# Performance work log

Hardware: AMD Instinct MI355X
Metric: run time of the kernel (lower is better)

The kernel has to match this reference:

```python
import jax, jax.numpy as jnp
import numpy as np

B, C, H, W = 2, 128, 64, 64
EPS = 1e-5


def setup_inputs() -> dict:
    key = jax.random.key(0)
    ks = jax.random.split(key, 8)
    sc = 1.0 / np.sqrt(C)
    inp = {
        "x": jax.random.normal(ks[0], (B, C, H, W, 2), jnp.float32),
        # naive complex BN affine params: per-channel, per-component (real/imag)
        "bn_w": jnp.ones((C, 2), jnp.float32),
        "bn_b": jnp.zeros((C, 2), jnp.float32),
        # complex 1x1 conv weights: (out_c, in_c, 2) -> [..,0]=W_real, [..,1]=W_imag
        "wq": jax.random.normal(ks[1], (C, C, 2), jnp.float32) * sc,
        "bq": jnp.zeros((C, 2), jnp.float32),
        "wk": jax.random.normal(ks[2], (C, C, 2), jnp.float32) * sc,
        "bk": jnp.zeros((C, 2), jnp.float32),
        "wv": jax.random.normal(ks[3], (C, C, 2), jnp.float32) * sc,
        "bv": jnp.zeros((C, 2), jnp.float32),
        "gamma": jnp.float32(0.05),
    }
    return inp


def _complex_bn(x, w, b):
    # naive complex BN: normalize real and imag independently per channel
    # x: (B,C,H,W,2); stats over (B,H,W) per (C, component)
    mean = x.mean(axis=(0, 2, 3), keepdims=True)
    var = x.var(axis=(0, 2, 3), keepdims=True)
    xn = (x - mean) * jax.lax.rsqrt(var + EPS)
    return xn * w[None, :, None, None, :] + b[None, :, None, None, :]


def _complex_conv1x1(x, w, b):
    # x: (B,C,H,W,2); w: (O,C,2); b: (O,2)
    xr, xi = x[..., 0], x[..., 1]
    wr, wi = w[..., 0], w[..., 1]
    yr = jnp.einsum('oc,bchw->bohw', wr, xr) - jnp.einsum('oc,bchw->bohw', wi, xi)
    yi = jnp.einsum('oc,bchw->bohw', wr, xi) + jnp.einsum('oc,bchw->bohw', wi, xr)
    yr = yr + b[:, 0][None, :, None, None]
    yi = yi + b[:, 1][None, :, None, None]
    return jnp.stack([yr, yi], axis=-1)


def _attention(x, wq, bq, wk, bk, wv, bv, gamma):
    scale = C ** (-0.5)
    N = H * W
    # q,k,v: (B,C,H,W,2) -> (B,C,N,2) -> (B,N,C,2)
    to_tokens = lambda t: t.reshape(B, C, N, 2).transpose(0, 2, 1, 3)
    q = to_tokens(_complex_conv1x1(x, wq, bq))
    k = to_tokens(_complex_conv1x1(x, wk, bk))
    v = to_tokens(_complex_conv1x1(x, wv, bv))

    qr, qi = q[..., 0], q[..., 1]          # (B,N,C)
    kr, ki = k[..., 0], -k[..., 1]         # conjugate of k
    # k_t = conj(k) with token/channel axes swapped -> (B,C,N)
    ktr = kr.transpose(0, 2, 1)
    kti = ki.transpose(0, 2, 1)

    # complex matmul q @ k_t -> only the real part is used downstream
    attn_real = jnp.einsum('bnc,bcm->bnm', qr, ktr) - jnp.einsum('bnc,bcm->bnm', qi, kti)
    attn_w = jax.nn.softmax(attn_real * scale, axis=-1)  # (B,N,N)
    # dropout = identity (eval mode)

    # attn is purely real -> complex matmul reduces to two real matmuls
    out_r = jnp.einsum('bnm,bmc->bnc', attn_w, v[..., 0])
    out_i = jnp.einsum('bnm,bmc->bnc', attn_w, v[..., 1])
    out = jnp.stack([out_r, out_i], axis=-1)              # (B,N,C,2)
    out = out.transpose(0, 2, 1, 3).reshape(B, C, H, W, 2)
    return x + gamma * out


def reference(x, bn_w, bn_b, wq, bq, wk, bk, wv, bv, gamma):
    xn = _complex_bn(x, bn_w, bn_b)
    return _attention(xn, wq, bq, wk, bk, wv, bv, gamma)
```

## Files before the change

kernel.cpp:

```cpp
#include <hip/hip_runtime.h>
#include <hip/hip_bf16.h>
#include <hip/hip_fp8.h>

typedef __bf16 bf16_t;
typedef __bf16 bf16x8 __attribute__((ext_vector_type(8)));
typedef float  f32x4  __attribute__((ext_vector_type(4)));
typedef long   i64_t;

#define MFMA16(A,B,C) __builtin_amdgcn_mfma_f32_16x16x32_bf16((A),(B),(C),0,0,0)
#define MFMA8(A,B,C)  __builtin_amdgcn_mfma_f32_16x16x32_fp8_fp8((A),(B),(C),0,0,0)
#define MFMA85(A,B,C) __builtin_amdgcn_mfma_f32_16x16x32_bf8_fp8((A),(B),(C),0,0,0)

constexpr int Bn = 2, Cc = 128, Hh = 64, Wd = 64;
constexpr int N  = Hh * Wd;
constexpr int T  = Bn * N;
constexpr int D  = 2 * Cc;
constexpr int NSP = 8;
constexpr float EPS = 1e-5f;
constexpr float SCL = 0.08838834764831845f * 1.4426950408889634f;
constexpr float PSH = 9.0f;

__device__ __forceinline__ int tfrag(int row, int ch) {
    return (((ch >> 5) * 4 + (row >> 4)) << 10) +
           ((((ch >> 3) & 3) * 16 + (row & 15)) << 4) + (ch & 7) * 2;
}
__device__ __forceinline__ int tfrag8(int row, int ch) {
    return (((ch >> 5) * 4 + (row >> 4)) << 9) +
           ((((ch >> 3) & 3) * 16 + (row & 15)) << 3) + (ch & 7);
}
__device__ __forceinline__ int vfrag8(int ch, int key) {
    return (((key >> 5) * 16 + (ch >> 4)) << 9) +
           ((((key >> 3) & 3) * 16 + (ch & 15)) << 3) + (key & 7);
}

__device__ __forceinline__ void gl16(const void* g, void* l) {
    __builtin_amdgcn_global_load_lds(
        (const __attribute__((address_space(1))) void*)g,
        (__attribute__((address_space(3))) void*)l, 16, 0, 0);
}

__global__ void k_pre(const float* __restrict__ x, float4* __restrict__ part,
                      const float* __restrict__ wq, const float* __restrict__ wk,
                      const float* __restrict__ wv, const float* __restrict__ bq,
                      const float* __restrict__ bk, const float* __restrict__ bv,
                      char* __restrict__ Wg, float* __restrict__ bt) {
    int tid = threadIdx.x;
    if (blockIdx.x < 512) {
        int bid = blockIdx.x;
        int q = bid >> 7, c = bid & 127;
        float sr = 0.f, si = 0.f, qr = 0.f, qi = 0.f;
        for (int b = 0; b < Bn; ++b) {
            const float2* p = (const float2*)x + (size_t)(b * Cc + c) * N + q * 1024;
            for (int i = tid; i < 1024; i += 256) {
                float2 v = p[i];
                sr += v.x; si += v.y; qr += v.x * v.x; qi += v.y * v.y;
            }
        }
        #pragma unroll
        for (int d = 32; d >= 1; d >>= 1) {
            sr += __shfl_xor(sr, d); si += __shfl_xor(si, d);
            qr += __shfl_xor(qr, d); qi += __shfl_xor(qi, d);
        }
        __shared__ float red[4][4];
        int w = tid >> 6;
        if ((tid & 63) == 0) { red[w][0] = sr; red[w][1] = si; red[w][2] = qr; red[w][3] = qi; }
        __syncthreads();
        if (tid == 0) {
            part[c * 4 + q] = make_float4(red[0][0] + red[1][0] + red[2][0] + red[3][0],
                                          red[0][1] + red[1][1] + red[2][1] + red[3][1],
                                          red[0][2] + red[1][2] + red[2][2] + red[3][2],
                                          red[0][3] + red[1][3] + red[2][3] + red[3][3]);
        }
    } else {
        int o = blockIdx.x - 512;
        int k = tid;
        int proj = o >> 8, oc = o & 255;
        const float* wsrc = proj == 0 ? wq : (proj == 1 ? wk : wv);
        const float* bsrc = proj == 0 ? bq : (proj == 1 ? bk : bv);
        int co = oc >> 7, oo = oc & 127;
        int c = k & 127, kc = k >> 7;
        float val;
        if (co == 0) val = (kc == 0) ? wsrc[(oo * 128 + c) * 2 + 0] : -wsrc[(oo * 128 + c) * 2 + 1];
        else         val = (kc == 0) ? wsrc[(oo * 128 + c) * 2 + 1] :  wsrc[(oo * 128 + c) * 2 + 0];
        int tile = o >> 6, row = o & 63;
        *(bf16_t*)(Wg + (size_t)tile * 32768 + tfrag(row, k)) = (bf16_t)val;
        if (k == 0) bt[o] = bsrc[oo * 2 + co];
    }
}

__global__ void k_norm(const float* __restrict__ x, const float4* __restrict__ part,
                       const float* __restrict__ bn_w, const float* __restrict__ bn_b,
                       char* __restrict__ XNg) {
    __shared__ float4 ssl[128];
    __shared__ __align__(16) char Tsh[32768];
    int blk = blockIdx.x;
    int b = blk >> 6, hw0 = (blk & 63) * 64;
    int tid = threadIdx.x;
    if (tid < 128) {
        float4 p0 = part[tid * 4 + 0], p1 = part[tid * 4 + 1];
        float4 p2 = part[tid * 4 + 2], p3 = part[tid * 4 + 3];
        float sr = p0.x + p1.x + p2.x + p3.x, si = p0.y + p1.y + p2.y + p3.y;
        float qr = p0.z + p1.z + p2.z + p3.z, qi = p0.w + p1.w + p2.w + p3.w;
        const float inv = 1.0f / (float)(Bn * N);
        float mr = sr * inv, mi = si * inv;
        float vr = qr * inv - mr * mr, vi = qi * inv - mi * mi;
        float scr = bn_w[tid * 2 + 0] * rsqrtf(vr + EPS);
        float sci = bn_w[tid * 2 + 1] * rsqrtf(vi + EPS);
        ssl[tid] = make_float4(scr, bn_b[tid * 2 + 0] - mr * scr,
                               sci, bn_b[tid * 2 + 1] - mi * sci);
    }
    __syncthreads();
    const float2* xin = (const float2*)x;
    #pragma unroll
    for (int it = 0; it < 32; ++it) {
        int idx = it * 256 + tid;
        int c = idx >> 6, hw = idx & 63;
        size_t gi = (size_t)(b * Cc + c) * N + hw0 + hw;
        float2 v = xin[gi];
        float4 s = ssl[c];
        *(bf16_t*)(Tsh + tfrag(hw, c))       = (bf16_t)(v.x * s.x + s.y);
        *(bf16_t*)(Tsh + tfrag(hw, c + 128)) = (bf16_t)(v.y * s.z + s.w);
    }
    __syncthreads();
    #pragma unroll
    for (int it = 0; it < 8; ++it) {
        int idx = it * 256 + tid;
        *(uint4*)(XNg + (size_t)blk * 32768 + idx * 16) = *(const uint4*)(Tsh + idx * 16);
    }
}

__global__ __launch_bounds__(256) void k_qkv(const char* __restrict__ XNg,
        const char* __restrict__ Wg, const float* __restrict__ bt,
        char* __restrict__ Qg, char* __restrict__ Kg, char* __restrict__ Vg) {
    __shared__ __align__(16) char Xsh[32768];
    __shared__ __align__(16) char Wsh[32768];
    int mx = blockIdx.x, ny = blockIdx.y;
    int tid = threadIdx.x;
    int w = tid >> 6, lane = tid & 63, n15 = lane & 15, quad = lane >> 4;
    const char* xs = XNg + (size_t)mx * 32768;
    const char* wsp = Wg + (size_t)ny * 32768;
    #pragma unroll
    for (int i = 0; i < 8; ++i) {
        int off = (w * 8 + i) * 1024 + lane * 16;
        gl16(xs + off, Xsh + off);
        gl16(wsp + off, Wsh + off);
    }
    __syncthreads();
    f32x4 acc[4] = {};
    #pragma unroll
    for (int ks = 0; ks < 8; ++ks) {
        bf16x8 a = *(const bf16x8*)(Xsh + (ks * 4 + w) * 1024 + lane * 16);
        #pragma unroll
        for (int t = 0; t < 4; ++t) {
            bf16x8 bw = *(const bf16x8*)(Wsh + (ks * 4 + t) * 1024 + lane * 16);
            acc[t] = MFMA16(a, bw, acc[t]);
        }
    }
    int proj = ny >> 2;
    int jb = (ny & 3) * 64;
    #pragma unroll
    for (int t = 0; t < 4; ++t) {
        int j = jb + t * 16 + n15;
        float bias = bt[ny * 64 + t * 16 + n15];
        unsigned w01 = (unsigned)__builtin_amdgcn_cvt_pk_fp8_f32(
            acc[t][0] + bias, acc[t][1] + bias, 0, false);
        unsigned w23 = (unsigned)__builtin_amdgcn_cvt_pk_fp8_f32(
            acc[t][2] + bias, acc[t][3] + bias, 0, false);
        #pragma unroll
        for (int r = 0; r < 4; ++r) {
            int tk = mx * 64 + w * 16 + quad * 4 + r;
            unsigned char v8 = (unsigned char)((r < 2 ? (w01 >> (8 * r))
                                                      : (w23 >> (8 * (r - 2)))) & 0xff);
            int bb = tk >> 12, n = tk & (N - 1);
            if (proj == 0) {
                *(unsigned char*)(Qg + (size_t)(tk >> 6) * 16384 + tfrag8(tk & 63, j)) = v8;
            } else {
                size_t tb = (size_t)(bb * 64 + (n >> 6)) * 16384;
                if (proj == 1) *(unsigned char*)(Kg + tb + tfrag8(n & 63, j)) = v8;
                else           *(unsigned char*)(Vg + tb + vfrag8(j, n & 63)) = v8;
            }
        }
    }
}

__global__ __launch_bounds__(256, 4) void k_attn(const char* __restrict__ Qg,
        const char* __restrict__ Kg, const char* __restrict__ Vg,
        bf16_t* __restrict__ Opb, float* __restrict__ Lp) {
    __shared__ __align__(16) char Ksh[16384];
    __shared__ __align__(16) char Vsh[16384];
    __shared__ __align__(16) char Psh[4096];
    int bid = blockIdx.x;
    int grp = bid & 15, qt = bid >> 4;
    int sp = grp & 7, b = grp >> 3;
    int tid = threadIdx.x;
    int w = tid >> 6, lane = tid & 63, n15 = lane & 15, quad = lane >> 4;
    int r = w >> 1, h = w & 1;

    const i64_t ONES = 0x3838383838383838L;

    i64_t qf[2][8];
    const char* qb = Qg + (size_t)(b * 64 + qt) * 16384;
    #pragma unroll
    for (int g = 0; g < 2; ++g)
        #pragma unroll
        for (int ks = 0; ks < 8; ++ks)
            qf[g][ks] = *(const i64_t*)(qb + ((ks * 4 + r * 2 + g) << 9) + lane * 8);

    f32x4 o[2][8] = {};
    f32x4 l_[2] = {};

    for (int kt = 0; kt < 8; ++kt) {
        size_t tb = (size_t)(b * 64 + sp * 8 + kt) * 16384;
        __syncthreads();
        #pragma unroll
        for (int i = 0; i < 4; ++i) {
            int off = (w * 4 + i) * 1024 + lane * 16;
            gl16(Kg + tb + off, Ksh + off);
            gl16(Vg + tb + off, Vsh + off);
        }
        __syncthreads();

        f32x4 s[2][2] = {};
        #pragma unroll
        for (int ks = 0; ks < 8; ++ks) {
            #pragma unroll
            for (int c = 0; c < 2; ++c) {
                i64_t kf = *(const i64_t*)(Ksh + ((ks * 4 + h * 2 + c) << 9) + lane * 8);
                s[0][c] = MFMA8(qf[0][ks], kf, s[0][c]);
                s[1][c] = MFMA8(qf[1][ks], kf, s[1][c]);
            }
        }
        #pragma unroll
        for (int g = 0; g < 2; ++g)
            #pragma unroll
            for (int c = 0; c < 2; ++c) {
                float p0 = __builtin_amdgcn_exp2f(s[g][c][0] * SCL - PSH);
                float p1 = __builtin_amdgcn_exp2f(s[g][c][1] * SCL - PSH);
                float p2 = __builtin_amdgcn_exp2f(s[g][c][2] * SCL - PSH);
                float p3 = __builtin_amdgcn_exp2f(s[g][c][3] * SCL - PSH);
                unsigned w01 = (unsigned)__builtin_amdgcn_cvt_pk_bf8_f32(p0, p1, 0, false);
                unsigned w23 = (unsigned)__builtin_amdgcn_cvt_pk_bf8_f32(p2, p3, 0, false);
                char* pb = Psh + ((h * 4 + r * 2 + g) << 9) +
                           (((c * 2 + (n15 >> 3)) * 16 + quad * 4) << 3) + (n15 & 7);
                pb[0]  = (unsigned char)(w01 & 0xff);
                pb[8]  = (unsigned char)((w01 >> 8) & 0xff);
                pb[16] = (unsigned char)(w23 & 0xff);
                pb[24] = (unsigned char)((w23 >> 8) & 0xff);
            }
        __syncthreads();

        #pragma unroll
        for (int k2 = 0; k2 < 2; ++k2) {
            i64_t pa0 = *(const i64_t*)(Psh + ((k2 * 4 + r * 2 + 0) << 9) + lane * 8);
            i64_t pa1 = *(const i64_t*)(Psh + ((k2 * 4 + r * 2 + 1) << 9) + lane * 8);
            l_[0] = MFMA85(pa0, ONES, l_[0]);
            l_[1] = MFMA85(pa1, ONES, l_[1]);
            #pragma unroll
            for (int ct = 0; ct < 8; ++ct) {
                i64_t vf = *(const i64_t*)(Vsh + ((k2 * 16 + h * 8 + ct) << 9) + lane * 8);
                o[0][ct] = MFMA85(pa0, vf, o[0][ct]);
                o[1][ct] = MFMA85(pa1, vf, o[1][ct]);
            }
        }
    }
    int tok0 = b * N + qt * 64 + r * 32;
    #pragma unroll
    for (int g = 0; g < 2; ++g) {
        #pragma unroll
        for (int ct = 0; ct < 8; ++ct)
            #pragma unroll
            for (int ri = 0; ri < 4; ++ri)
                Opb[((size_t)sp * T + tok0 + g * 16 + quad * 4 + ri) * D +
                    h * 128 + ct * 16 + n15] = (bf16_t)o[g][ct][ri];
        if (h == 0 && n15 == 0) {
            #pragma unroll
            for (int ri = 0; ri < 4; ++ri)
                Lp[sp * T + tok0 + g * 16 + quad * 4 + ri] = l_[g][ri];
        }
    }
}

__global__ void k_comb(const bf16_t* __restrict__ Opb, const float* __restrict__ Lp,
                       const float4* __restrict__ part, const float* __restrict__ bn_w,
                       const float* __restrict__ bn_b, const float* __restrict__ x,
                       const float* __restrict__ gamma, float* __restrict__ out) {
    __shared__ float4 ssl[128];
    __shared__ float wts[32];
    __shared__ float Ot[256 * 33];
    int blk = blockIdx.x;
    int b = blk >> 7, hw0 = (blk & 127) * 32;
    int tok0 = b * N + hw0;
    int tid = threadIdx.x;
    if (tid < 128) {
        float4 p0 = part[tid * 4 + 0], p1 = part[tid * 4 + 1];
        float4 p2 = part[tid * 4 + 2], p3 = part[tid * 4 + 3];
        float sr = p0.x + p1.x + p2.x + p3.x, si = p0.y + p1.y + p2.y + p3.y;
        float qr = p0.z + p1.z + p2.z + p3.z, qi = p0.w + p1.w + p2.w + p3.w;
        const float inv = 1.0f / (float)(Bn * N);
        float mr = sr * inv, mi = si * inv;
        float vr = qr * inv - mr * mr, vi = qi * inv - mi * mi;
        float scr = bn_w[tid * 2 + 0] * rsqrtf(vr + EPS);
        float sci = bn_w[tid * 2 + 1] * rsqrtf(vi + EPS);
        ssl[tid] = make_float4(scr, bn_b[tid * 2 + 0] - mr * scr,
                               sci, bn_b[tid * 2 + 1] - mi * sci);
    }
    if (tid < 32) {
        float Z = 0.f;
        #pragma unroll
        for (int s = 0; s < NSP; ++s) Z += Lp[s * T + tok0 + tid];
        wts[tid] = gamma[0] / Z;
    }
    __syncthreads();
    #pragma unroll
    for (int i = 0; i < 4; ++i) {
        int idx = i * 256 + tid;
        int tk = idx >> 5, chunk = idx & 31;
        size_t base = (size_t)(tok0 + tk) * D + chunk * 8;
        float acc[8] = {};
        #pragma unroll
        for (int s = 0; s < NSP; ++s) {
            bf16x8 v = *(const bf16x8*)(Opb + (size_t)s * T * D + base);
            #pragma unroll
            for (int j = 0; j < 8; ++j) acc[j] += (float)v[j];
        }
        float ww = wts[tk];
        #pragma unroll
        for (int j = 0; j < 8; ++j) Ot[(chunk * 8 + j) * 33 + tk] = acc[j] * ww;
    }
    __syncthreads();
    const float2* xin = (const float2*)x;
    float2* xo = (float2*)out;
    #pragma unroll
    for (int i = 0; i < 16; ++i) {
        int linear = i * 256 + tid;
        int c = linear >> 5, hwo = linear & 31;
        size_t idx = (size_t)(b * Cc + c) * N + hw0 + hwo;
        float2 v = xin[idx];
        float4 s = ssl[c];
        float2 res;
        res.x = v.x * s.x + s.y + Ot[c * 33 + hwo];
        res.y = v.y * s.z + s.w + Ot[(128 + c) * 33 + hwo];
        xo[idx] = res;
    }
}

extern "C" void kernel_launch(void* const* d_in, const int* in_sizes, int n_in,
                              void* d_out, int out_size, void* d_ws, size_t ws_size,
                              hipStream_t stream) {
    const float* x    = (const float*)d_in[0];
    const float* bn_w = (const float*)d_in[1];
    const float* bn_b = (const float*)d_in[2];
    const float* wq   = (const float*)d_in[3];
    const float* bq   = (const float*)d_in[4];
    const float* wk   = (const float*)d_in[5];
    const float* bk   = (const float*)d_in[6];
    const float* wv   = (const float*)d_in[7];
    const float* bv   = (const float*)d_in[8];
    const float* gam  = (const float*)d_in[9];
    float* out = (float*)d_out;

    char* ws = (char*)d_ws;
    size_t off = 0;
    auto alloc = [&](size_t bytes) -> void* {
        void* p = ws + off;
        off += (bytes + 255) & ~(size_t)255;
        return p;
    };
    float4* part = (float4*)alloc(512 * sizeof(float4));
    char*   XNg  = (char*)alloc((size_t)128 * 32768);
    char*   Wg   = (char*)alloc((size_t)12 * 32768);
    float*  bt   = (float*)alloc(768 * 4);
    char*   Qg   = (char*)alloc((size_t)128 * 16384);
    char*   Kg   = (char*)alloc((size_t)128 * 16384);
    char*   Vg   = (char*)alloc((size_t)128 * 16384);
    bf16_t* Opb  = (bf16_t*)alloc((size_t)NSP * T * D * 2);
    float*  Lp   = (float*)alloc((size_t)NSP * T * 4);

    k_pre<<<1280, 256, 0, stream>>>(x, part, wq, wk, wv, bq, bk, bv, Wg, bt);
    k_norm<<<128, 256, 0, stream>>>(x, part, bn_w, bn_b, XNg);
    k_qkv<<<dim3(128, 12), 256, 0, stream>>>(XNg, Wg, bt, Qg, Kg, Vg);
    k_attn<<<1024, 256, 0, stream>>>(Qg, Kg, Vg, Opb, Lp);
    k_comb<<<256, 256, 0, stream>>>(Opb, Lp, part, bn_w, bn_b, x, gam, out);
}
```

Before: 149.7 us.

## Halve attention key splits, stage QKV stores in LDS, vectorize x loads

Reduces the key-dimension split count for attention from 8 to 4, so each attention block processes 16 key tiles and the combine kernel reads fewer partial outputs. The QKV projection now writes fp8 results into shared memory first and then emits coalesced 16-byte global stores, replacing scattered single-byte writes. The stats and normalization kernels load x as float4 instead of float2. The combine kernel is retiled to 16 tokens per block with 512 blocks. Fewer splits means fewer attention blocks (512), which lowers parallelism per wave but cuts partial-sum traffic.

```diff
diff --git a/kernel.cpp b/kernel.cpp
--- a/kernel.cpp
+++ b/kernel.cpp
@@ -15,7 +15,7 @@
 constexpr int N  = Hh * Wd;
 constexpr int T  = Bn * N;
 constexpr int D  = 2 * Cc;
-constexpr int NSP = 8;
+constexpr int NSP = 4;
 constexpr float EPS = 1e-5f;
 constexpr float SCL = 0.08838834764831845f * 1.4426950408889634f;
 constexpr float PSH = 9.0f;
@@ -23,14 +23,6 @@
 __device__ __forceinline__ int tfrag(int row, int ch) {
     return (((ch >> 5) * 4 + (row >> 4)) << 10) +
            ((((ch >> 3) & 3) * 16 + (row & 15)) << 4) + (ch & 7) * 2;
-}
-__device__ __forceinline__ int tfrag8(int row, int ch) {
-    return (((ch >> 5) * 4 + (row >> 4)) << 9) +
-           ((((ch >> 3) & 3) * 16 + (row & 15)) << 3) + (ch & 7);
-}
-__device__ __forceinline__ int vfrag8(int ch, int key) {
-    return (((key >> 5) * 16 + (ch >> 4)) << 9) +
-           ((((key >> 3) & 3) * 16 + (ch & 15)) << 3) + (key & 7);
 }
 
 __device__ __forceinline__ void gl16(const void* g, void* l) {
@@ -50,10 +42,12 @@
         int q = bid >> 7, c = bid & 127;
         float sr = 0.f, si = 0.f, qr = 0.f, qi = 0.f;
         for (int b = 0; b < Bn; ++b) {
-            const float2* p = (const float2*)x + (size_t)(b * Cc + c) * N + q * 1024;
-            for (int i = tid; i < 1024; i += 256) {
-                float2 v = p[i];
-                sr += v.x; si += v.y; qr += v.x * v.x; qi += v.y * v.y;
+            const float4* p = (const float4*)((const float2*)x +
+                              (size_t)(b * Cc + c) * N + q * 1024);
+            for (int i = tid; i < 512; i += 256) {
+                float4 v = p[i];
+                sr += v.x + v.z; si += v.y + v.w;
+                qr += v.x * v.x + v.z * v.z; qi += v.y * v.y + v.w * v.w;
             }
         }
         #pragma unroll
@@ -110,16 +104,18 @@
                                sci, bn_b[tid * 2 + 1] - mi * sci);
     }
     __syncthreads();
-    const float2* xin = (const float2*)x;
-    #pragma unroll
-    for (int it = 0; it < 32; ++it) {
+    const float4* xin4 = (const float4*)x;
+    #pragma unroll
+    for (int it = 0; it < 16; ++it) {
         int idx = it * 256 + tid;
-        int c = idx >> 6, hw = idx & 63;
-        size_t gi = (size_t)(b * Cc + c) * N + hw0 + hw;
-        float2 v = xin[gi];
+        int c = idx >> 5, h2 = (idx & 31) * 2;
+        size_t gi = ((size_t)(b * Cc + c) * N + hw0 + h2) >> 1;
+        float4 v = xin4[gi];
         float4 s = ssl[c];
-        *(bf16_t*)(Tsh + tfrag(hw, c))       = (bf16_t)(v.x * s.x + s.y);
-        *(bf16_t*)(Tsh + tfrag(hw, c + 128)) = (bf16_t)(v.y * s.z + s.w);
+        *(bf16_t*)(Tsh + tfrag(h2, c))           = (bf16_t)(v.x * s.x + s.y);
+        *(bf16_t*)(Tsh + tfrag(h2, c + 128))     = (bf16_t)(v.y * s.z + s.w);
+        *(bf16_t*)(Tsh + tfrag(h2 + 1, c))       = (bf16_t)(v.z * s.x + s.y);
+        *(bf16_t*)(Tsh + tfrag(h2 + 1, c + 128)) = (bf16_t)(v.w * s.z + s.w);
     }
     __syncthreads();
     #pragma unroll
@@ -158,28 +154,41 @@
     }
     int proj = ny >> 2;
     int jb = (ny & 3) * 64;
+    __syncthreads();
+    char* Osh = Xsh;
     #pragma unroll
     for (int t = 0; t < 4; ++t) {
-        int j = jb + t * 16 + n15;
         float bias = bt[ny * 64 + t * 16 + n15];
         unsigned w01 = (unsigned)__builtin_amdgcn_cvt_pk_fp8_f32(
             acc[t][0] + bias, acc[t][1] + bias, 0, false);
         unsigned w23 = (unsigned)__builtin_amdgcn_cvt_pk_fp8_f32(
             acc[t][2] + bias, acc[t][3] + bias, 0, false);
+        unsigned char vb[4] = {(unsigned char)(w01 & 0xff), (unsigned char)((w01 >> 8) & 0xff),
+                               (unsigned char)(w23 & 0xff), (unsigned char)((w23 >> 8) & 0xff)};
         #pragma unroll
         for (int r = 0; r < 4; ++r) {
-            int tk = mx * 64 + w * 16 + quad * 4 + r;
-            unsigned char v8 = (unsigned char)((r < 2 ? (w01 >> (8 * r))
-                                                      : (w23 >> (8 * (r - 2)))) & 0xff);
-            int bb = tk >> 12, n = tk & (N - 1);
-            if (proj == 0) {
-                *(unsigned char*)(Qg + (size_t)(tk >> 6) * 16384 + tfrag8(tk & 63, j)) = v8;
+            if (proj < 2) {
+                int lf  = (t >> 1) * 4 + w;
+                int lif = (((2 * t + (n15 >> 3)) & 3) << 4) + quad * 4 + r;
+                Osh[lf * 512 + lif * 8 + (n15 & 7)] = vb[r];
             } else {
-                size_t tb = (size_t)(bb * 64 + (n >> 6)) * 16384;
-                if (proj == 1) *(unsigned char*)(Kg + tb + tfrag8(n & 63, j)) = v8;
-                else           *(unsigned char*)(Vg + tb + vfrag8(j, n & 63)) = v8;
-            }
-        }
+                int key = w * 16 + quad * 4 + r;
+                int lf  = (w >> 1) * 4 + t;
+                int lif = (((key >> 3) & 3) << 4) + n15;
+                Osh[lf * 512 + lif * 8 + (key & 7)] = vb[r];
+            }
+        }
+    }
+    __syncthreads();
+    {
+        int lf = tid >> 5, sub = (tid & 31) * 16;
+        size_t tile = (proj == 0) ? (size_t)mx
+                                  : (size_t)((mx >> 6) * 64 + (mx & 63));
+        int gfrag = (proj < 2) ? ((jb >> 5) * 4 + lf)
+                               : ((lf >> 2) * 16 + (jb >> 4) + (lf & 3));
+        char* dst = (proj == 0 ? Qg : (proj == 1 ? Kg : Vg));
+        *(uint4*)(dst + tile * 16384 + (size_t)gfrag * 512 + sub) =
+            *(const uint4*)(Osh + tid * 16);
     }
 }
 
@@ -190,8 +199,8 @@
     __shared__ __align__(16) char Vsh[16384];
     __shared__ __align__(16) char Psh[4096];
     int bid = blockIdx.x;
-    int grp = bid & 15, qt = bid >> 4;
-    int sp = grp & 7, b = grp >> 3;
+    int grp = bid & 7, qt = bid >> 3;
+    int sp = grp & 3, b = grp >> 2;
     int tid = threadIdx.x;
     int w = tid >> 6, lane = tid & 63, n15 = lane & 15, quad = lane >> 4;
     int r = w >> 1, h = w & 1;
@@ -209,8 +218,8 @@
     f32x4 o[2][8] = {};
     f32x4 l_[2] = {};
 
-    for (int kt = 0; kt < 8; ++kt) {
-        size_t tb = (size_t)(b * 64 + sp * 8 + kt) * 16384;
+    for (int kt = 0; kt < 16; ++kt) {
+        size_t tb = (size_t)(b * 64 + sp * 16 + kt) * 16384;
         __syncthreads();
         #pragma unroll
         for (int i = 0; i < 4; ++i) {
@@ -285,10 +294,10 @@
                        const float* __restrict__ bn_b, const float* __restrict__ x,
                        const float* __restrict__ gamma, float* __restrict__ out) {
     __shared__ float4 ssl[128];
-    __shared__ float wts[32];
-    __shared__ float Ot[256 * 33];
+    __shared__ float wts[16];
+    __shared__ float Ot[256 * 17];
     int blk = blockIdx.x;
-    int b = blk >> 7, hw0 = (blk & 127) * 32;
+    int b = blk >> 8, hw0 = (blk & 255) * 16;
     int tok0 = b * N + hw0;
     int tid = threadIdx.x;
     if (tid < 128) {
@@ -304,7 +313,7 @@
         ssl[tid] = make_float4(scr, bn_b[tid * 2 + 0] - mr * scr,
                                sci, bn_b[tid * 2 + 1] - mi * sci);
     }
-    if (tid < 32) {
+    if (tid < 16) {
         float Z = 0.f;
         #pragma unroll
         for (int s = 0; s < NSP; ++s) Z += Lp[s * T + tok0 + tid];
@@ -312,7 +321,7 @@
     }
     __syncthreads();
     #pragma unroll
-    for (int i = 0; i < 4; ++i) {
+    for (int i = 0; i < 2; ++i) {
         int idx = i * 256 + tid;
         int tk = idx >> 5, chunk = idx & 31;
         size_t base = (size_t)(tok0 + tk) * D + chunk * 8;
@@ -325,21 +334,21 @@
         }
         float ww = wts[tk];
         #pragma unroll
-        for (int j = 0; j < 8; ++j) Ot[(chunk * 8 + j) * 33 + tk] = acc[j] * ww;
+        for (int j = 0; j < 8; ++j) Ot[(chunk * 8 + j) * 17 + tk] = acc[j] * ww;
     }
     __syncthreads();
     const float2* xin = (const float2*)x;
     float2* xo = (float2*)out;
     #pragma unroll
-    for (int i = 0; i < 16; ++i) {
+    for (int i = 0; i < 8; ++i) {
         int linear = i * 256 + tid;
-        int c = linear >> 5, hwo = linear & 31;
+        int c = linear >> 4, hwo = linear & 15;
         size_t idx = (size_t)(b * Cc + c) * N + hw0 + hwo;
         float2 v = xin[idx];
         float4 s = ssl[c];
         float2 res;
-        res.x = v.x * s.x + s.y + Ot[c * 33 + hwo];
-        res.y = v.y * s.z + s.w + Ot[(128 + c) * 33 + hwo];
+        res.x = v.x * s.x + s.y + Ot[c * 17 + hwo];
+        res.y = v.y * s.z + s.w + Ot[(128 + c) * 17 + hwo];
         xo[idx] = res;
     }
 }
@@ -379,6 +388,6 @@
     k_pre<<<1280, 256, 0, stream>>>(x, part, wq, wk, wv, bq, bk, bv, Wg, bt);
     k_norm<<<128, 256, 0, stream>>>(x, part, bn_w, bn_b, XNg);
     k_qkv<<<dim3(128, 12), 256, 0, stream>>>(XNg, Wg, bt, Qg, Kg, Vg);
-    k_attn<<<1024, 256, 0, stream>>>(Qg, Kg, Vg, Opb, Lp);
-    k_comb<<<256, 256, 0, stream>>>(Opb, Lp, part, bn_w, bn_b, x, gam, out);
-}
+    k_attn<<<512, 256, 0, stream>>>(Qg, Kg, Vg, Opb, Lp);
+    k_comb<<<512, 256, 0, stream>>>(Opb, Lp, part, bn_w, bn_b, x, gam, out);
+}
```

After: 150.0 us. No clear change (+0.2%).
